# Performance work log

Measured on AMD Instinct MI355X. Metric: run time of the kernel, lower is better.

Reference implementation:

```python
import jax, jax.numpy as jnp
import numpy as np

B, S, D, H = 4, 2048, 1024, 16
DK = D // H


def setup_inputs() -> dict:
    key = jax.random.key(0)
    ks = jax.random.split(key, 12)
    std = 0.02
    inp = {
        "query": jax.random.normal(ks[0], (B, S, D), jnp.float32),
        "key": jax.random.normal(ks[1], (B, S, D), jnp.float32),
        "value": jax.random.normal(ks[2], (B, S, D), jnp.float32),
        "mask": jnp.ones((B, 1, 1, S), jnp.int32),
        "Wq": jax.random.normal(ks[3], (D, D), jnp.float32) * std,
        "bq": jnp.zeros((D,), jnp.float32),
        "Wk": jax.random.normal(ks[4], (D, D), jnp.float32) * std,
        "bk": jnp.zeros((D,), jnp.float32),
        "Wv": jax.random.normal(ks[5], (D, D), jnp.float32) * std,
        "bv": jnp.zeros((D,), jnp.float32),
        "Wo": jax.random.normal(ks[6], (D, D), jnp.float32) * std,
        "bo": jnp.zeros((D,), jnp.float32),
    }
    return inp


def reference(query, key, value, mask, Wq, bq, Wk, bk, Wv, bv, Wo, bo):
    # nn.Linear: x @ W.T + b; then split heads -> [B, H, S, DK]
    def proj(x, W, b):
        y = x @ W.T + b
        return y.reshape(B, S, H, DK).transpose(0, 2, 1, 3)

    q = proj(query, Wq, bq)
    k = proj(key, Wk, bk)
    v = proj(value, Wv, bv)

    scale = 1.0 / jnp.sqrt(jnp.asarray(DK, q.dtype))
    scores = jnp.einsum('bhqd,bhkd->bhqk', q, k) * scale  # [B,H,S,S]
    scores = jnp.where(mask == 0, jnp.asarray(-1e9, scores.dtype), scores)
    p_attn = jax.nn.softmax(scores, axis=-1)  # dropout p=0 -> identity
    ctx = jnp.einsum('bhqk,bhkd->bhqd', p_attn, v)
    ctx = ctx.transpose(0, 2, 1, 3).reshape(B, S, D)
    out = ctx @ Wo.T + bo
    return out
```

## Files before the change

kernel.cpp:

```cpp
#include <hip/hip_runtime.h>

#define BB 4
#define SS 2048
#define DD 1024
#define HH 16
#define DKC 64
#define MT (BB*SS)

typedef _Float16 f16x8 __attribute__((ext_vector_type(8)));
typedef _Float16 f16x4 __attribute__((ext_vector_type(4)));
typedef float f32x4 __attribute__((ext_vector_type(4)));
typedef int   i32x4 __attribute__((ext_vector_type(4)));

typedef __attribute__((address_space(1))) void GV;
typedef __attribute__((address_space(3))) void LV;

__device__ __forceinline__ void async_copy16(const void* g, void* l) {
  __builtin_amdgcn_global_load_lds((GV*)g, (LV*)l, 16, 0, 0);
}

__global__ __launch_bounds__(256) void cvt3(const float* __restrict__ s0,
                                            const float* __restrict__ s1,
                                            const float* __restrict__ s2,
                                            _Float16* __restrict__ dst, int n) {
  const float* src = (blockIdx.y == 0) ? s0 : ((blockIdx.y == 1) ? s1 : s2);
  _Float16* d = dst + (size_t)blockIdx.y * n;
  int i = (blockIdx.x * 256 + threadIdx.x) * 4;
  if (i < n) {
    f32x4 f = *(const f32x4*)(src + i);
    f16x4 o;
#pragma unroll
    for (int j = 0; j < 4; ++j) o[j] = (_Float16)f[j];
    *(f16x4*)(d + i) = o;
  }
}

__global__ __launch_bounds__(256) void cvt4(const float* __restrict__ s0,
                                            const float* __restrict__ s1,
                                            const float* __restrict__ s2,
                                            const float* __restrict__ s3,
                                            _Float16* __restrict__ dst, int n) {
  const float* src = (blockIdx.y == 0) ? s0 : ((blockIdx.y == 1) ? s1 :
                     ((blockIdx.y == 2) ? s2 : s3));
  _Float16* d = dst + (size_t)blockIdx.y * n;
  int i = (blockIdx.x * 256 + threadIdx.x) * 4;
  if (i < n) {
    f32x4 f = *(const f32x4*)(src + i);
    f16x4 o;
#pragma unroll
    for (int j = 0; j < 4; ++j) o[j] = (_Float16)f[j];
    *(f16x4*)(d + i) = o;
  }
}

__global__ __launch_bounds__(256) void gemm_qkv(const _Float16* __restrict__ Xb,
                                                const _Float16* __restrict__ Wb,
                                                const float* __restrict__ b0,
                                                const float* __restrict__ b1,
                                                const float* __restrict__ b2,
                                                _Float16* __restrict__ Pj) {
  const int z = blockIdx.z;
  const _Float16* A = Xb + (size_t)z * MT * DD;
  const _Float16* W = Wb + (size_t)z * DD * DD;
  const float* bias = (z == 0) ? b0 : ((z == 1) ? b1 : b2);
  _Float16* out = Pj + (size_t)z * MT * DD;

  const int m0 = blockIdx.y * 128;
  const int n0 = blockIdx.x * 128;
  const int t = threadIdx.x;
  const int lane = t & 63;
  const int wave = t >> 6;
  const int q = lane >> 4, r = lane & 15;
  const int wm = (wave & 1) * 64, wn = (wave >> 1) * 64;

  __shared__ __align__(16) _Float16 sA[128 * 32];
  __shared__ __align__(16) _Float16 sB[128 * 32];

  f32x4 acc[4][4] = {};

  for (int k0 = 0; k0 < DD; k0 += 32) {
#pragma unroll
    for (int i = 0; i < 2; ++i) {
      int c = t + 256 * i;
      int row = c >> 2, cc = c & 3;
      async_copy16(A + (size_t)(m0 + row) * DD + k0 + cc * 8, &sA[c * 8]);
      async_copy16(W + (size_t)(n0 + row) * DD + k0 + cc * 8, &sB[c * 8]);
    }
    __syncthreads();
    f16x8 af[4], bf[4];
#pragma unroll
    for (int x = 0; x < 4; ++x) {
      af[x] = *(const f16x8*)&sA[(wm + x * 16 + r) * 32 + q * 8];
      bf[x] = *(const f16x8*)&sB[(wn + x * 16 + r) * 32 + q * 8];
    }
#pragma unroll
    for (int mi = 0; mi < 4; ++mi)
#pragma unroll
      for (int ni = 0; ni < 4; ++ni)
        acc[mi][ni] = __builtin_amdgcn_mfma_f32_16x16x32_f16(af[mi], bf[ni], acc[mi][ni], 0, 0, 0);
    __syncthreads();
  }

  if (z == 2) {
#pragma unroll
    for (int ni = 0; ni < 4; ++ni) {
      int gn = n0 + wn + ni * 16 + r;
      float bv = bias[gn];
      int h = gn >> 6, dk = gn & 63;
#pragma unroll
      for (int mi = 0; mi < 4; ++mi) {
        int gm = m0 + wm + mi * 16 + q * 4;
        int bb = gm >> 11, s = gm & 2047;
        f16x4 o4;
#pragma unroll
        for (int rr = 0; rr < 4; ++rr) o4[rr] = (_Float16)(acc[mi][ni][rr] + bv);
        *(f16x4*)&out[((size_t)((bb * HH + h) * DKC + dk)) * SS + s] = o4;
      }
    }
  } else {
#pragma unroll
    for (int ni = 0; ni < 4; ++ni) {
      int gn = n0 + wn + ni * 16 + r;
      float bv = bias[gn];
      int h = gn >> 6, dk = gn & 63;
#pragma unroll
      for (int mi = 0; mi < 4; ++mi) {
#pragma unroll
        for (int rr = 0; rr < 4; ++rr) {
          int gm = m0 + wm + mi * 16 + q * 4 + rr;
          int bb = gm >> 11, s = gm & 2047;
          out[((size_t)((bb * HH + h) * SS + s)) * DKC + dk] = (_Float16)(acc[mi][ni][rr] + bv);
        }
      }
    }
  }
}

__global__ __launch_bounds__(256) void attn(const _Float16* __restrict__ Pj,
                                            const int* __restrict__ mask,
                                            _Float16* __restrict__ Cx) {
  const int qt = blockIdx.x, h = blockIdx.y, bb = blockIdx.z;
  const size_t hoff = ((size_t)(bb * HH + h) * SS) * DKC;
  const _Float16* Qh  = Pj + hoff;
  const _Float16* Kh  = Pj + (size_t)MT * DD + hoff;
  const _Float16* Vth = Pj + (size_t)2 * MT * DD + hoff;
  _Float16* Ch = Cx + hoff;
  const int* mrow = mask + bb * SS;

  const int t = threadIdx.x, lane = t & 63, wave = t >> 6;
  const int q = lane >> 4, r = lane & 15;
  const int qrow0 = qt * 128 + wave * 32;

  __shared__ __align__(16) _Float16 sK[64 * 64];
  __shared__ __align__(16) _Float16 sVt[64 * 64];
  __shared__ __align__(16) _Float16 sP[4][32 * 64];
  __shared__ __align__(16) float    sMB[SS];

  {
    int i0 = t * 8;
    i32x4 m0v = *(const i32x4*)(mrow + i0);
    i32x4 m1v = *(const i32x4*)(mrow + i0 + 4);
    f32x4 b0v, b1v;
#pragma unroll
    for (int j = 0; j < 4; ++j) {
      b0v[j] = m0v[j] ? 0.0f : -1e30f;
      b1v[j] = m1v[j] ? 0.0f : -1e30f;
    }
    *(f32x4*)&sMB[i0] = b0v;
    *(f32x4*)&sMB[i0 + 4] = b1v;
  }

  f16x8 qf[2][2];
#pragma unroll
  for (int mi = 0; mi < 2; ++mi)
#pragma unroll
    for (int kk = 0; kk < 2; ++kk)
      qf[mi][kk] = *(const f16x8*)&Qh[(size_t)(qrow0 + mi * 16 + r) * DKC + kk * 32 + q * 8];

  float lst[2][4] = {};
  f32x4 oacc[2][4] = {};

  const float C2 = 0.125f * 1.44269504089f;

  const int srow0 = t >> 3, scc = t & 7;

  f16x8 kpre[2], vpre[2];
#pragma unroll
  for (int i = 0; i < 2; ++i) {
    int row = srow0 + 32 * i;
    kpre[i] = *(const f16x8*)(Kh + (size_t)row * DKC + scc * 8);
    vpre[i] = *(const f16x8*)(Vth + (size_t)row * SS + scc * 8);
  }

  for (int kt = 0; kt < SS; kt += 64) {
#pragma unroll
    for (int i = 0; i < 2; ++i) {
      int row = srow0 + 32 * i;
      int off = row * 64 + (((scc ^ (row & 7)) << 3));
      *(f16x8*)&sK [off] = kpre[i];
      *(f16x8*)&sVt[off] = vpre[i];
    }
    __syncthreads();

    if (kt + 64 < SS) {
#pragma unroll
      for (int i = 0; i < 2; ++i) {
        int row = srow0 + 32 * i;
        kpre[i] = *(const f16x8*)(Kh + (size_t)(kt + 64 + row) * DKC + scc * 8);
        vpre[i] = *(const f16x8*)(Vth + (size_t)row * SS + kt + 64 + scc * 8);
      }
    }

    f32x4 sacc[2][4] = {};
#pragma unroll
    for (int kk = 0; kk < 2; ++kk) {
      f16x8 kb[4];
#pragma unroll
      for (int ni = 0; ni < 4; ++ni)
        kb[ni] = *(const f16x8*)&sK[(ni * 16 + r) * 64 + ((((kk * 4 + q) ^ (r & 7)) << 3))];
#pragma unroll
      for (int mi = 0; mi < 2; ++mi)
#pragma unroll
        for (int ni = 0; ni < 4; ++ni)
          sacc[mi][ni] = __builtin_amdgcn_mfma_f32_16x16x32_f16(qf[mi][kk], kb[ni], sacc[mi][ni], 0, 0, 0);
    }

    float mb[4];
#pragma unroll
    for (int ni = 0; ni < 4; ++ni) mb[ni] = sMB[kt + ni * 16 + r];

#pragma unroll
    for (int mi = 0; mi < 2; ++mi) {
#pragma unroll
      for (int rr = 0; rr < 4; ++rr) {
        int rowoff = (mi * 16 + q * 4 + rr) * 64;
        int ksw = ((q << 1) | (rr & 1)) << 3;
#pragma unroll
        for (int ni = 0; ni < 4; ++ni) {
          float p = __builtin_amdgcn_exp2f(__builtin_fmaf(sacc[mi][ni][rr], C2, mb[ni]));
          lst[mi][rr] += p;
          sP[wave][rowoff + ((ni * 16 + r) ^ ksw)] = (_Float16)p;
        }
      }
    }
    __threadfence_block();

#pragma unroll
    for (int kk = 0; kk < 2; ++kk) {
      f16x8 ap[2], vb[4];
#pragma unroll
      for (int mi = 0; mi < 2; ++mi) {
        int row = mi * 16 + r;
        int ksw = ((((r >> 2) & 3) << 1) | (r & 1)) << 3;
        ap[mi] = *(const f16x8*)&sP[wave][row * 64 + ((kk * 32 + q * 8) ^ ksw)];
      }
#pragma unroll
      for (int ni = 0; ni < 4; ++ni) {
        vb[ni] = *(const f16x8*)&sVt[(ni * 16 + r) * 64 + ((((kk * 4 + q) ^ (r & 7)) << 3))];
      }
#pragma unroll
      for (int mi = 0; mi < 2; ++mi)
#pragma unroll
        for (int ni = 0; ni < 4; ++ni)
          oacc[mi][ni] = __builtin_amdgcn_mfma_f32_16x16x32_f16(ap[mi], vb[ni], oacc[mi][ni], 0, 0, 0);
    }
    __syncthreads();
  }

#pragma unroll
  for (int mi = 0; mi < 2; ++mi)
#pragma unroll
    for (int rr = 0; rr < 4; ++rr) {
      float l = lst[mi][rr];
#pragma unroll
      for (int d = 1; d < 16; d <<= 1) l += __shfl_xor(l, d);
      lst[mi][rr] = 1.0f / l;
    }

#pragma unroll
  for (int mi = 0; mi < 2; ++mi)
#pragma unroll
    for (int ni = 0; ni < 4; ++ni)
#pragma unroll
      for (int rr = 0; rr < 4; ++rr) {
        int row = qrow0 + mi * 16 + q * 4 + rr;
        Ch[(size_t)row * DKC + ni * 16 + r] = (_Float16)(oacc[mi][ni][rr] * lst[mi][rr]);
      }
}

__global__ __launch_bounds__(256) void gemm_out(const _Float16* __restrict__ Cx,
                                                const _Float16* __restrict__ W,
                                                const float* __restrict__ bias,
                                                float* __restrict__ out) {
  const int m0 = blockIdx.y * 128;
  const int n0 = blockIdx.x * 128;
  const int t = threadIdx.x;
  const int lane = t & 63;
  const int wave = t >> 6;
  const int q = lane >> 4, r = lane & 15;
  const int wm = (wave & 1) * 64, wn = (wave >> 1) * 64;

  __shared__ __align__(16) _Float16 sA[128 * 32];
  __shared__ __align__(16) _Float16 sB[128 * 32];

  f32x4 acc[4][4] = {};

  for (int k0 = 0; k0 < DD; k0 += 32) {
#pragma unroll
    for (int i = 0; i < 2; ++i) {
      int c = t + 256 * i;
      int row = c >> 2, cc = c & 3;
      int gm = m0 + row;
      int bb = gm >> 11, s = gm & 2047;
      int head = k0 >> 6, off = (k0 & 63) + cc * 8;
      async_copy16(Cx + ((size_t)(bb * HH + head) * SS + s) * DKC + off, &sA[c * 8]);
      async_copy16(W + (size_t)(n0 + row) * DD + k0 + cc * 8, &sB[c * 8]);
    }
    __syncthreads();
    f16x8 af[4], bf[4];
#pragma unroll
    for (int x = 0; x < 4; ++x) {
      af[x] = *(const f16x8*)&sA[(wm + x * 16 + r) * 32 + q * 8];
      bf[x] = *(const f16x8*)&sB[(wn + x * 16 + r) * 32 + q * 8];
    }
#pragma unroll
    for (int mi = 0; mi < 4; ++mi)
#pragma unroll
      for (int ni = 0; ni < 4; ++ni)
        acc[mi][ni] = __builtin_amdgcn_mfma_f32_16x16x32_f16(af[mi], bf[ni], acc[mi][ni], 0, 0, 0);
    __syncthreads();
  }

#pragma unroll
  for (int ni = 0; ni < 4; ++ni) {
    int gn = n0 + wn + ni * 16 + r;
    float bv = bias[gn];
#pragma unroll
    for (int mi = 0; mi < 4; ++mi) {
#pragma unroll
      for (int rr = 0; rr < 4; ++rr) {
        int gm = m0 + wm + mi * 16 + q * 4 + rr;
        out[(size_t)gm * DD + gn] = acc[mi][ni][rr] + bv;
      }
    }
  }
}

extern "C" void kernel_launch(void* const* d_in, const int* in_sizes, int n_in,
                              void* d_out, int out_size, void* d_ws, size_t ws_size,
                              hipStream_t stream) {
  const float* query = (const float*)d_in[0];
  const float* key_  = (const float*)d_in[1];
  const float* value = (const float*)d_in[2];
  const int*   mask  = (const int*)d_in[3];
  const float* Wq = (const float*)d_in[4];
  const float* bq = (const float*)d_in[5];
  const float* Wk = (const float*)d_in[6];
  const float* bk = (const float*)d_in[7];
  const float* Wv = (const float*)d_in[8];
  const float* bv = (const float*)d_in[9];
  const float* Wo = (const float*)d_in[10];
  const float* bo = (const float*)d_in[11];
  float* out = (float*)d_out;

  const int nX = MT * DD;
  const int nW = DD * DD;

  _Float16* Xb = (_Float16*)d_ws;
  _Float16* Wb = Xb + (size_t)3 * nX;
  _Float16* Pj = Wb + (size_t)4 * nW;
  _Float16* Cx = Pj + (size_t)3 * nX;

  cvt3<<<dim3(nX / 1024, 3), 256, 0, stream>>>(query, key_, value, Xb, nX);
  cvt4<<<dim3(nW / 1024, 4), 256, 0, stream>>>(Wq, Wk, Wv, Wo, Wb, nW);

  gemm_qkv<<<dim3(DD / 128, MT / 128, 3), 256, 0, stream>>>(Xb, Wb, bq, bk, bv, Pj);
  attn<<<dim3(SS / 128, HH, BB), 256, 0, stream>>>(Pj, mask, Cx);
  gemm_out<<<dim3(DD / 128, MT / 128), 256, 0, stream>>>(Cx, Wb + (size_t)3 * nW, bo, out);
}
```

Baseline: 386.2 us.

## Register-prefetch next K tile in projection GEMMs and swap grid block order

Replaces the direct global-to-LDS async copies in both projection GEMMs with a register double-buffer. The next K slice is loaded into registers while MFMAs run on the current LDS tile, then stored to LDS at the top of the next iteration. The grid is also transposed so consecutive blocks walk the M dimension and share the same weight column tile, which changes L2 reuse. This costs extra VGPRs and a register-to-LDS store pass, and gives up the hardware direct-to-LDS load path.

```diff
diff --git a/kernel.cpp b/kernel.cpp
--- a/kernel.cpp
+++ b/kernel.cpp
@@ -11,13 +11,6 @@
 typedef _Float16 f16x4 __attribute__((ext_vector_type(4)));
 typedef float f32x4 __attribute__((ext_vector_type(4)));
 typedef int   i32x4 __attribute__((ext_vector_type(4)));
-
-typedef __attribute__((address_space(1))) void GV;
-typedef __attribute__((address_space(3))) void LV;
-
-__device__ __forceinline__ void async_copy16(const void* g, void* l) {
-  __builtin_amdgcn_global_load_lds((GV*)g, (LV*)l, 16, 0, 0);
-}
 
 __global__ __launch_bounds__(256) void cvt3(const float* __restrict__ s0,
                                             const float* __restrict__ s1,
@@ -65,8 +58,8 @@
   const float* bias = (z == 0) ? b0 : ((z == 1) ? b1 : b2);
   _Float16* out = Pj + (size_t)z * MT * DD;
 
-  const int m0 = blockIdx.y * 128;
-  const int n0 = blockIdx.x * 128;
+  const int m0 = blockIdx.x * 128;
+  const int n0 = blockIdx.y * 128;
   const int t = threadIdx.x;
   const int lane = t & 63;
   const int wave = t >> 6;
@@ -78,15 +71,34 @@
 
   f32x4 acc[4][4] = {};
 
+  const int row0 = t >> 2, cc = t & 3;
+
+  f16x8 apre[2], bpre[2];
+#pragma unroll
+  for (int i = 0; i < 2; ++i) {
+    int row = row0 + 64 * i;
+    apre[i] = *(const f16x8*)(A + (size_t)(m0 + row) * DD + cc * 8);
+    bpre[i] = *(const f16x8*)(W + (size_t)(n0 + row) * DD + cc * 8);
+  }
+
   for (int k0 = 0; k0 < DD; k0 += 32) {
 #pragma unroll
     for (int i = 0; i < 2; ++i) {
       int c = t + 256 * i;
-      int row = c >> 2, cc = c & 3;
-      async_copy16(A + (size_t)(m0 + row) * DD + k0 + cc * 8, &sA[c * 8]);
-      async_copy16(W + (size_t)(n0 + row) * DD + k0 + cc * 8, &sB[c * 8]);
-    }
-    __syncthreads();
+      *(f16x8*)&sA[c * 8] = apre[i];
+      *(f16x8*)&sB[c * 8] = bpre[i];
+    }
+    __syncthreads();
+
+    if (k0 + 32 < DD) {
+#pragma unroll
+      for (int i = 0; i < 2; ++i) {
+        int row = row0 + 64 * i;
+        apre[i] = *(const f16x8*)(A + (size_t)(m0 + row) * DD + k0 + 32 + cc * 8);
+        bpre[i] = *(const f16x8*)(W + (size_t)(n0 + row) * DD + k0 + 32 + cc * 8);
+      }
+    }
+
     f16x8 af[4], bf[4];
 #pragma unroll
     for (int x = 0; x < 4; ++x) {
@@ -292,8 +304,8 @@
                                                 const _Float16* __restrict__ W,
                                                 const float* __restrict__ bias,
                                                 float* __restrict__ out) {
-  const int m0 = blockIdx.y * 128;
-  const int n0 = blockIdx.x * 128;
+  const int m0 = blockIdx.x * 128;
+  const int n0 = blockIdx.y * 128;
   const int t = threadIdx.x;
   const int lane = t & 63;
   const int wave = t >> 6;
@@ -305,18 +317,41 @@
 
   f32x4 acc[4][4] = {};
 
+  const int row0 = t >> 2, cc = t & 3;
+  size_t abase[2];
+#pragma unroll
+  for (int i = 0; i < 2; ++i) {
+    int gm = m0 + row0 + 64 * i;
+    int bb = gm >> 11, s = gm & 2047;
+    abase[i] = ((size_t)(bb * HH) * SS + s) * DKC;
+  }
+
+  f16x8 apre[2], bpre[2];
+#pragma unroll
+  for (int i = 0; i < 2; ++i) {
+    apre[i] = *(const f16x8*)(Cx + abase[i] + cc * 8);
+    bpre[i] = *(const f16x8*)(W + (size_t)(n0 + row0 + 64 * i) * DD + cc * 8);
+  }
+
   for (int k0 = 0; k0 < DD; k0 += 32) {
 #pragma unroll
     for (int i = 0; i < 2; ++i) {
       int c = t + 256 * i;
-      int row = c >> 2, cc = c & 3;
-      int gm = m0 + row;
-      int bb = gm >> 11, s = gm & 2047;
-      int head = k0 >> 6, off = (k0 & 63) + cc * 8;
-      async_copy16(Cx + ((size_t)(bb * HH + head) * SS + s) * DKC + off, &sA[c * 8]);
-      async_copy16(W + (size_t)(n0 + row) * DD + k0 + cc * 8, &sB[c * 8]);
-    }
-    __syncthreads();
+      *(f16x8*)&sA[c * 8] = apre[i];
+      *(f16x8*)&sB[c * 8] = bpre[i];
+    }
+    __syncthreads();
+
+    if (k0 + 32 < DD) {
+      int k1 = k0 + 32;
+      int head = k1 >> 6, off = (k1 & 63) + cc * 8;
+#pragma unroll
+      for (int i = 0; i < 2; ++i) {
+        apre[i] = *(const f16x8*)(Cx + abase[i] + (size_t)head * SS * DKC + off);
+        bpre[i] = *(const f16x8*)(W + (size_t)(n0 + row0 + 64 * i) * DD + k1 + cc * 8);
+      }
+    }
+
     f16x8 af[4], bf[4];
 #pragma unroll
     for (int x = 0; x < 4; ++x) {
@@ -374,7 +409,7 @@
   cvt3<<<dim3(nX / 1024, 3), 256, 0, stream>>>(query, key_, value, Xb, nX);
   cvt4<<<dim3(nW / 1024, 4), 256, 0, stream>>>(Wq, Wk, Wv, Wo, Wb, nW);
 
-  gemm_qkv<<<dim3(DD / 128, MT / 128, 3), 256, 0, stream>>>(Xb, Wb, bq, bk, bv, Pj);
+  gemm_qkv<<<dim3(MT / 128, DD / 128, 3), 256, 0, stream>>>(Xb, Wb, bq, bk, bv, Pj);
   attn<<<dim3(SS / 128, HH, BB), 256, 0, stream>>>(Pj, mask, Cx);
-  gemm_out<<<dim3(DD / 128, MT / 128), 256, 0, stream>>>(Cx, Wb + (size_t)3 * nW, bo, out);
-}
+  gemm_out<<<dim3(MT / 128, DD / 128), 256, 0, stream>>>(Cx, Wb + (size_t)3 * nW, bo, out);
+}
```

Measured after the change: 382.0 us. Within noise of the previous version (-1.1%).
